# Optimization experiments

Hardware: AMD Instinct MI355X
Metric: run time of the kernel (lower is better)

The kernel has to match this reference:

```python
import jax, jax.numpy as jnp
import numpy as np
from jax import lax

H = 32   # hidden_size
L = 8    # num_layers
D_IN = 64    # lstm input_size / fc0 out
FEAT = 4096  # feature_size
T = 300      # frame_size
B = 64       # batch


def setup_inputs() -> dict:
    key = jax.random.key(0)
    ks = jax.random.split(key, 16)
    s = 0.05
    inp = {
        "x": jax.random.normal(ks[0], (B, T, FEAT), dtype=jnp.float32),
        # fc0: Linear(4096->64), ReLU, Dropout(eval), Linear(64->64)
        "W0": jax.random.normal(ks[1], (D_IN, FEAT), dtype=jnp.float32) * s,
        "b0": jax.random.normal(ks[2], (D_IN,), dtype=jnp.float32) * s,
        "W1": jax.random.normal(ks[3], (D_IN, D_IN), dtype=jnp.float32) * s,
        "b1": jax.random.normal(ks[4], (D_IN,), dtype=jnp.float32) * s,
        # LSTM params, PyTorch layout: W_ih [4H, in], W_hh [4H, H], biases [4H]
        "Wih0": jax.random.normal(ks[5], (4 * H, D_IN), dtype=jnp.float32) * s,
        "Wih": jax.random.normal(ks[6], (L - 1, 4 * H, H), dtype=jnp.float32) * s,
        "Whh": jax.random.normal(ks[7], (L, 4 * H, H), dtype=jnp.float32) * s,
        "bih": jax.random.normal(ks[8], (L, 4 * H), dtype=jnp.float32) * s,
        "bhh": jax.random.normal(ks[9], (L, 4 * H), dtype=jnp.float32) * s,
        # fc1: 32 -> 1 ; fc2: 300 -> 1
        "Wfc1": jax.random.normal(ks[10], (1, H), dtype=jnp.float32) * s,
        "bfc1": jax.random.normal(ks[11], (1,), dtype=jnp.float32) * s,
        "Wfc2": jax.random.normal(ks[12], (1, T), dtype=jnp.float32) * s,
        "bfc2": jax.random.normal(ks[13], (1,), dtype=jnp.float32) * s,
    }
    return inp


def _lstm_layer(x_seq, Wih_l, Whh_l, bih_l, bhh_l):
    # x_seq: [B, T, in] -> h_seq: [B, T, H]; PyTorch gate order i,f,g,o
    gx = jnp.einsum('bti,gi->btg', x_seq, Wih_l) + bih_l  # [B,T,4H]
    b = x_seq.shape[0]
    init = (jnp.zeros((b, H), x_seq.dtype), jnp.zeros((b, H), x_seq.dtype))

    def step(carry, gx_t):
        h, c = carry
        g = gx_t + h @ Whh_l.T + bhh_l
        i, f, gg, o = jnp.split(g, 4, axis=-1)
        c = jax.nn.sigmoid(f) * c + jax.nn.sigmoid(i) * jnp.tanh(gg)
        h = jax.nn.sigmoid(o) * jnp.tanh(c)
        return (h, c), h

    _, hs = lax.scan(step, init, jnp.swapaxes(gx, 0, 1))  # hs: [T,B,H]
    return jnp.swapaxes(hs, 0, 1)


def reference(x, W0, b0, W1, b1, Wih0, Wih, Whh, bih, bhh, Wfc1, bfc1, Wfc2, bfc2):
    # fc0 (dropout is identity in eval mode)
    h = jax.nn.relu(jnp.einsum('btf,of->bto', x, W0) + b0)
    h = jnp.einsum('bti,oi->bto', h, W1) + b1  # [B,T,64]
    # stacked LSTM, h0=c0=0
    for l in range(L):
        Wih_l = Wih0 if l == 0 else Wih[l - 1]
        h = _lstm_layer(h, Wih_l, Whh[l], bih[l], bhh[l])  # [B,T,32]
    # fc1 over hidden, squeeze, fc2 over time, squeeze
    y = jnp.einsum('bth,oh->bto', h, Wfc1)[..., 0] + bfc1[0]  # [B,T]
    y = y @ Wfc2.T + bfc2  # [B,1]
    return y[:, 0]
```

## Files before the change

kernel.cpp:

```cpp
#include <hip/hip_runtime.h>
#include <cstdint>

#define FEAT 4096
#define DIN  64
#define HS   32
#define NL   8
#define TT   300
#define BB   64
#define G4   128
#define MROWS (BB*TT)
#define KS    4
#define KSLICE (FEAT/KS)
#define BK    64
#define NCHUNK (KSLICE/BK)

typedef __bf16 bf16x8 __attribute__((ext_vector_type(8)));
typedef float  f32x4  __attribute__((ext_vector_type(4)));
typedef unsigned short u16x8 __attribute__((ext_vector_type(8)));

__device__ __forceinline__ float sigm(float x){ return __fdividef(1.f, 1.f + __expf(-x)); }
__device__ __forceinline__ float tanh_f(float x){ return __fdividef(2.f, 1.f + __expf(-2.f*x)) - 1.f; }

__device__ __forceinline__ unsigned short bf16_rne(float f){
    uint32_t u = __float_as_uint(f);
    return (unsigned short)((u + 0x7FFFu + ((u >> 16) & 1u)) >> 16);
}

__global__ __launch_bounds__(256) void w0split(const float* __restrict__ W0,
                                               unsigned short* __restrict__ wh,
                                               unsigned short* __restrict__ wl)
{
    const int i = (blockIdx.x * 256 + threadIdx.x) * 4;
    float4 v = *(const float4*)(W0 + i);
    float f[4] = {v.x, v.y, v.z, v.w};
    unsigned short hh[4], ll[4];
    #pragma unroll
    for (int j = 0; j < 4; ++j) {
        unsigned short h = bf16_rne(f[j]);
        float fh = __uint_as_float((uint32_t)h << 16);
        hh[j] = h;
        ll[j] = bf16_rne(f[j] - fh);
    }
    *(ushort4*)(wh + i) = make_ushort4(hh[0], hh[1], hh[2], hh[3]);
    *(ushort4*)(wl + i) = make_ushort4(ll[0], ll[1], ll[2], ll[3]);
}

__global__ __launch_bounds__(256, 2) void fc_gemm1(
    const float* __restrict__ x,
    const unsigned short* __restrict__ wh,
    const unsigned short* __restrict__ wl,
    float* __restrict__ part)
{
    __shared__ __align__(16) unsigned short xh[2][64][64];
    __shared__ __align__(16) unsigned short xl[2][64][64];
    __shared__ __align__(16) unsigned short wh_s[2][64][64];
    __shared__ __align__(16) unsigned short wl_s[2][64][64];

    const int t   = threadIdx.x;
    const int l   = t & 63;
    const int w   = t >> 6;
    const int rbb = (w >> 1) * 32;
    const int cbb = (w & 1) * 32;
    const int r0  = blockIdx.x * 64;
    const int kb0 = blockIdx.y * KSLICE;

    const int srow = t >> 3;
    const int sg   = t & 7;

    f32x4 acc[2][2];
    #pragma unroll
    for (int i = 0; i < 2; ++i)
        #pragma unroll
        for (int j = 0; j < 2; ++j)
            acc[i][j] = (f32x4){0.f, 0.f, 0.f, 0.f};

    float4 xr[2][2];
    uint4  w0h[2], w0l[2];

    auto LOAD = [&](int c) {
        const float* xb = x + (size_t)r0 * FEAT + kb0 + c * BK;
        xr[0][0] = *(const float4*)(xb + (size_t)srow * FEAT + sg * 8);
        xr[0][1] = *(const float4*)(xb + (size_t)srow * FEAT + sg * 8 + 4);
        xr[1][0] = *(const float4*)(xb + (size_t)(srow + 32) * FEAT + sg * 8);
        xr[1][1] = *(const float4*)(xb + (size_t)(srow + 32) * FEAT + sg * 8 + 4);
        const int wo = kb0 + c * BK + sg * 8;
        w0h[0] = *(const uint4*)(wh + (size_t)srow * FEAT + wo);
        w0h[1] = *(const uint4*)(wh + (size_t)(srow + 32) * FEAT + wo);
        w0l[0] = *(const uint4*)(wl + (size_t)srow * FEAT + wo);
        w0l[1] = *(const uint4*)(wl + (size_t)(srow + 32) * FEAT + wo);
    };

    auto STORE = [&](int c) {
        const int buf = c & 1;
        #pragma unroll
        for (int j = 0; j < 2; ++j) {
            const int row = srow + j * 32;
            const int gsw = (sg ^ (row & 7)) * 8;
            float f0[8] = {xr[j][0].x, xr[j][0].y, xr[j][0].z, xr[j][0].w,
                           xr[j][1].x, xr[j][1].y, xr[j][1].z, xr[j][1].w};
            u16x8 vh, vl;
            #pragma unroll
            for (int i = 0; i < 8; ++i) {
                uint32_t u  = __float_as_uint(f0[i]);
                uint32_t rh = (u + 0x7FFFu + ((u >> 16) & 1u)) >> 16;
                vh[i] = (unsigned short)rh;
                float fl = f0[i] - __uint_as_float(rh << 16);
                uint32_t u2 = __float_as_uint(fl);
                vl[i] = (unsigned short)((u2 + 0x7FFFu + ((u2 >> 16) & 1u)) >> 16);
            }
            *(u16x8*)&xh[buf][row][gsw] = vh;
            *(u16x8*)&xl[buf][row][gsw] = vl;
            *(uint4*)&wh_s[buf][row][gsw] = w0h[j];
            *(uint4*)&wl_s[buf][row][gsw] = w0l[j];
        }
    };

    auto COMPUTE = [&](int buf) {
        #pragma unroll
        for (int kstep = 0; kstep < 2; ++kstep) {
            const int gA = kstep * 4 + (l >> 4);
            bf16x8 Ah[2], Al[2], Bh[2], Bl[2];
            #pragma unroll
            for (int rf = 0; rf < 2; ++rf) {
                const int ra  = rbb + rf * 16 + (l & 15);
                const int off = (gA ^ (ra & 7)) * 8;
                Ah[rf] = __builtin_bit_cast(bf16x8, *(const u16x8*)&xh[buf][ra][off]);
                Al[rf] = __builtin_bit_cast(bf16x8, *(const u16x8*)&xl[buf][ra][off]);
            }
            #pragma unroll
            for (int cf = 0; cf < 2; ++cf) {
                const int cb  = cbb + cf * 16 + (l & 15);
                const int off = (gA ^ (cb & 7)) * 8;
                Bh[cf] = __builtin_bit_cast(bf16x8, *(const u16x8*)&wh_s[buf][cb][off]);
                Bl[cf] = __builtin_bit_cast(bf16x8, *(const u16x8*)&wl_s[buf][cb][off]);
            }
            #pragma unroll
            for (int rf = 0; rf < 2; ++rf)
                #pragma unroll
                for (int cf = 0; cf < 2; ++cf) {
                    acc[rf][cf] = __builtin_amdgcn_mfma_f32_16x16x32_bf16(Ah[rf], Bh[cf], acc[rf][cf], 0, 0, 0);
                    acc[rf][cf] = __builtin_amdgcn_mfma_f32_16x16x32_bf16(Al[rf], Bh[cf], acc[rf][cf], 0, 0, 0);
                    acc[rf][cf] = __builtin_amdgcn_mfma_f32_16x16x32_bf16(Ah[rf], Bl[cf], acc[rf][cf], 0, 0, 0);
                }
        }
    };

    LOAD(0);
    for (int c = 0; c < NCHUNK; ++c) {
        STORE(c);
        if (c + 1 < NCHUNK) LOAD(c + 1);
        asm volatile("s_waitcnt lgkmcnt(0)" ::: "memory");
        __builtin_amdgcn_s_barrier();
        COMPUTE(c & 1);
    }

    #pragma unroll
    for (int rf = 0; rf < 2; ++rf)
        #pragma unroll
        for (int cf = 0; cf < 2; ++cf)
            #pragma unroll
            for (int r = 0; r < 4; ++r) {
                const int row = r0 + rbb + rf * 16 + (l >> 4) * 4 + r;
                const int col = cbb + cf * 16 + (l & 15);
                part[((size_t)blockIdx.y * MROWS + row) * 64 + col] = acc[rf][cf][r];
            }
}

__global__ __launch_bounds__(256) void fc_tail(
    const float* __restrict__ part, const float* __restrict__ b0,
    const float* __restrict__ W1, const float* __restrict__ b1,
    const float* __restrict__ Wih0,
    const float* __restrict__ bih, const float* __restrict__ bhh,
    float* __restrict__ gx0)
{
    __shared__ __align__(16) float h1s[64][68];
    __shared__ __align__(16) float h2s[64][68];

    const int tid = threadIdx.x;
    const int tc  = tid & 15;
    const int tr  = tid >> 4;
    const int r0  = blockIdx.x * 64;

    {
        const int row = tid >> 2;
        const int c0  = (tid & 3) * 16;
        float4 s[4];
        #pragma unroll
        for (int i = 0; i < 4; ++i)
            s[i] = *(const float4*)(part + ((size_t)(r0 + row)) * 64 + c0 + 4 * i);
        #pragma unroll
        for (int ks = 1; ks < KS; ++ks)
            #pragma unroll
            for (int i = 0; i < 4; ++i) {
                float4 v = *(const float4*)(part + ((size_t)ks * MROWS + r0 + row) * 64 + c0 + 4 * i);
                s[i].x += v.x; s[i].y += v.y; s[i].z += v.z; s[i].w += v.w;
            }
        #pragma unroll
        for (int i = 0; i < 4; ++i) {
            float4 bv = *(const float4*)(b0 + c0 + 4 * i);
            float4 o;
            o.x = fmaxf(s[i].x + bv.x, 0.f);
            o.y = fmaxf(s[i].y + bv.y, 0.f);
            o.z = fmaxf(s[i].z + bv.z, 0.f);
            o.w = fmaxf(s[i].w + bv.w, 0.f);
            *(float4*)&h1s[row][c0 + 4 * i] = o;
        }
    }
    __syncthreads();

    float acc2[4][4] = {};
    #pragma unroll
    for (int k4 = 0; k4 < 16; ++k4) {
        const int k = k4 * 4;
        float4 a[4], wv[4];
        #pragma unroll
        for (int i = 0; i < 4; ++i) a[i] = *(const float4*)&h1s[tr * 4 + i][k];
        #pragma unroll
        for (int j = 0; j < 4; ++j) wv[j] = *(const float4*)(W1 + (size_t)(tc * 4 + j) * DIN + k);
        #pragma unroll
        for (int i = 0; i < 4; ++i)
            #pragma unroll
            for (int j = 0; j < 4; ++j)
                acc2[i][j] += a[i].x * wv[j].x + a[i].y * wv[j].y + a[i].z * wv[j].z + a[i].w * wv[j].w;
    }
    __syncthreads();
    #pragma unroll
    for (int i = 0; i < 4; ++i)
        #pragma unroll
        for (int j = 0; j < 4; ++j)
            h2s[tr * 4 + i][tc * 4 + j] = acc2[i][j] + b1[tc * 4 + j];
    __syncthreads();

    #pragma unroll
    for (int p = 0; p < 2; ++p) {
        float acc3[4][4] = {};
        #pragma unroll
        for (int k4 = 0; k4 < 16; ++k4) {
            const int k = k4 * 4;
            float4 a[4], wv[4];
            #pragma unroll
            for (int i = 0; i < 4; ++i) a[i] = *(const float4*)&h2s[tr * 4 + i][k];
            #pragma unroll
            for (int j = 0; j < 4; ++j) wv[j] = *(const float4*)(Wih0 + (size_t)(p * 64 + tc * 4 + j) * DIN + k);
            #pragma unroll
            for (int i = 0; i < 4; ++i)
                #pragma unroll
                for (int j = 0; j < 4; ++j)
                    acc3[i][j] += a[i].x * wv[j].x + a[i].y * wv[j].y + a[i].z * wv[j].z + a[i].w * wv[j].w;
        }
        const int g0 = p * 64 + tc * 4;
        #pragma unroll
        for (int i = 0; i < 4; ++i) {
            float4 ov;
            ov.x = acc3[i][0] + bih[g0 + 0] + bhh[g0 + 0];
            ov.y = acc3[i][1] + bih[g0 + 1] + bhh[g0 + 1];
            ov.z = acc3[i][2] + bih[g0 + 2] + bhh[g0 + 2];
            ov.w = acc3[i][3] + bih[g0 + 3] + bhh[g0 + 3];
            *(float4*)(gx0 + (size_t)(r0 + tr * 4 + i) * G4 + g0) = ov;
        }
    }
}

__global__ __launch_bounds__(512, 2) void lstm_all(
    const float* __restrict__ gx0,
    const float* __restrict__ Wih, const float* __restrict__ Whh,
    const float* __restrict__ bih, const float* __restrict__ bhh,
    const float* __restrict__ Wfc1, const float* __restrict__ bfc1,
    const float* __restrict__ Wfc2, const float* __restrict__ bfc2,
    float* __restrict__ out)
{
    const int b    = blockIdx.x;
    const int tid  = threadIdx.x;
    const int l    = tid >> 6;
    const int lane = tid & 63;
    const int q0   = lane;
    const int q1   = lane + 64;

    __shared__ __align__(16) float hbuf[NL][2][HS];
    __shared__ __align__(16) float gbuf[NL][G4];
    __shared__ __align__(16) float h7[TT][HS];
    __shared__ float red[NL];

    float whh0[HS], whh1[HS], wih0[HS], wih1[HS];
    {
        const float* whhl = Whh + (size_t)l * G4 * HS;
        const float* wihl = Wih + (size_t)(l > 0 ? l - 1 : 0) * G4 * HS;
        #pragma unroll
        for (int k4 = 0; k4 < 8; ++k4) {
            float4 v0 = *(const float4*)(whhl + q0 * HS + 4 * k4);
            float4 v1 = *(const float4*)(whhl + q1 * HS + 4 * k4);
            whh0[4*k4+0]=v0.x; whh0[4*k4+1]=v0.y; whh0[4*k4+2]=v0.z; whh0[4*k4+3]=v0.w;
            whh1[4*k4+0]=v1.x; whh1[4*k4+1]=v1.y; whh1[4*k4+2]=v1.z; whh1[4*k4+3]=v1.w;
            float4 u0 = *(const float4*)(wihl + q0 * HS + 4 * k4);
            float4 u1 = *(const float4*)(wihl + q1 * HS + 4 * k4);
            wih0[4*k4+0]=u0.x; wih0[4*k4+1]=u0.y; wih0[4*k4+2]=u0.z; wih0[4*k4+3]=u0.w;
            wih1[4*k4+0]=u1.x; wih1[4*k4+1]=u1.y; wih1[4*k4+2]=u1.z; wih1[4*k4+3]=u1.w;
        }
    }
    const float bias0 = (l > 0) ? (bih[l*G4 + q0] + bhh[l*G4 + q0]) : 0.f;
    const float bias1 = (l > 0) ? (bih[l*G4 + q1] + bhh[l*G4 + q1]) : 0.f;

    float c_state = 0.f;

    const float* gxb = gx0 + (size_t)b * TT * G4;
    float pf0 = 0.f, pf1 = 0.f;
    if (l == 0) { pf0 = gxb[q0]; pf1 = gxb[q1]; }

    for (int s = 0; s < TT + NL - 1; ++s) {
        const int t = s - l;
        if (0 <= t && t < TT) {
            float acc0, acc1;
            if (l == 0) {
                acc0 = pf0; acc1 = pf1;
                const int tn = t + 1;
                if (tn < TT) { pf0 = gxb[(size_t)tn * G4 + q0]; pf1 = gxb[(size_t)tn * G4 + q1]; }
            } else {
                acc0 = bias0; acc1 = bias1;
            }
            float a0a = 0.f, a0b = 0.f, a1a = 0.f, a1b = 0.f;
            if (t > 0) {
                const float4* hp = (const float4*)hbuf[l][(t - 1) & 1];
                #pragma unroll
                for (int k4 = 0; k4 < 8; ++k4) {
                    float4 v = hp[k4];
                    a0a = fmaf(whh0[4*k4+0], v.x, a0a); a0b = fmaf(whh0[4*k4+1], v.y, a0b);
                    a0a = fmaf(whh0[4*k4+2], v.z, a0a); a0b = fmaf(whh0[4*k4+3], v.w, a0b);
                    a1a = fmaf(whh1[4*k4+0], v.x, a1a); a1b = fmaf(whh1[4*k4+1], v.y, a1b);
                    a1a = fmaf(whh1[4*k4+2], v.z, a1a); a1b = fmaf(whh1[4*k4+3], v.w, a1b);
                }
            }
            if (l > 0) {
                const float4* hq = (const float4*)hbuf[l - 1][t & 1];
                #pragma unroll
                for (int k4 = 0; k4 < 8; ++k4) {
                    float4 v = hq[k4];
                    a0a = fmaf(wih0[4*k4+0], v.x, a0a); a0b = fmaf(wih0[4*k4+1], v.y, a0b);
                    a0a = fmaf(wih0[4*k4+2], v.z, a0a); a0b = fmaf(wih0[4*k4+3], v.w, a0b);
                    a1a = fmaf(wih1[4*k4+0], v.x, a1a); a1b = fmaf(wih1[4*k4+1], v.y, a1b);
                    a1a = fmaf(wih1[4*k4+2], v.z, a1a); a1b = fmaf(wih1[4*k4+3], v.w, a1b);
                }
            }
            acc0 += a0a + a0b;
            acc1 += a1a + a1b;
            gbuf[l][q0] = acc0;
            gbuf[l][q1] = acc1;
            asm volatile("s_waitcnt lgkmcnt(0)" ::: "memory");
            if (lane < HS) {
                const float ig = gbuf[l][lane];
                const float fg = gbuf[l][HS + lane];
                const float gg = gbuf[l][2*HS + lane];
                const float og = gbuf[l][3*HS + lane];
                c_state = sigm(fg) * c_state + sigm(ig) * tanh_f(gg);
                const float hv = sigm(og) * tanh_f(c_state);
                hbuf[l][t & 1][lane] = hv;
                if (l == NL - 1) h7[t][lane] = hv;
            }
        }
        __syncthreads();
    }

    float part = 0.f;
    for (int t = tid; t < TT; t += 512) {
        float st = 0.f;
        #pragma unroll
        for (int j = 0; j < HS; ++j) st = fmaf(h7[t][j], Wfc1[j], st);
        part += (st + bfc1[0]) * Wfc2[t];
    }
    #pragma unroll
    for (int off = 32; off >= 1; off >>= 1) part += __shfl_down(part, off, 64);
    if (lane == 0) red[l] = part;
    __syncthreads();
    if (tid == 0) {
        float tot = 0.f;
        #pragma unroll
        for (int w = 0; w < NL; ++w) tot += red[w];
        out[b] = tot + bfc2[0];
    }
}

extern "C" void kernel_launch(void* const* d_in, const int* in_sizes, int n_in,
                              void* d_out, int out_size, void* d_ws, size_t ws_size,
                              hipStream_t stream) {
    const float* x    = (const float*)d_in[0];
    const float* W0   = (const float*)d_in[1];
    const float* b0   = (const float*)d_in[2];
    const float* W1   = (const float*)d_in[3];
    const float* b1   = (const float*)d_in[4];
    const float* Wih0 = (const float*)d_in[5];
    const float* Wih  = (const float*)d_in[6];
    const float* Whh  = (const float*)d_in[7];
    const float* bih  = (const float*)d_in[8];
    const float* bhh  = (const float*)d_in[9];
    const float* Wfc1 = (const float*)d_in[10];
    const float* bfc1 = (const float*)d_in[11];
    const float* Wfc2 = (const float*)d_in[12];
    const float* bfc2 = (const float*)d_in[13];

    char* wsb = (char*)d_ws;
    float*          gx0 = (float*)wsb;
    unsigned short* wh  = (unsigned short*)(wsb + 9830400);
    unsigned short* wl  = (unsigned short*)(wsb + 9830400 + 524288);
    float*          prt = (float*)(wsb + 9830400 + 1048576);

    w0split <<<256, 256, 0, stream>>>(W0, wh, wl);
    fc_gemm1<<<dim3(MROWS / 64, KS), 256, 0, stream>>>(x, wh, wl, prt);
    fc_tail <<<MROWS / 64, 256, 0, stream>>>(prt, b0, W1, b1, Wih0, bih, bhh, gx0);
    lstm_all<<<BB, 512, 0, stream>>>(gx0, Wih, Whh, bih, bhh, Wfc1, bfc1, Wfc2, bfc2,
                                     (float*)d_out);
}
```

Measured before the change: 432.3 us.

## Process two timesteps per barrier in wavefront LSTM and use shuffle gate exchange

```diff
diff --git a/kernel.cpp b/kernel.cpp
--- a/kernel.cpp
+++ b/kernel.cpp
@@ -13,6 +13,7 @@
 #define KSLICE (FEAT/KS)
 #define BK    64
 #define NCHUNK (KSLICE/BK)
+#define NSUP  (TT/2 + NL - 1)
 
 typedef __bf16 bf16x8 __attribute__((ext_vector_type(8)));
 typedef float  f32x4  __attribute__((ext_vector_type(4)));
@@ -20,6 +21,13 @@
 
 __device__ __forceinline__ float sigm(float x){ return __fdividef(1.f, 1.f + __expf(-x)); }
 __device__ __forceinline__ float tanh_f(float x){ return __fdividef(2.f, 1.f + __expf(-2.f*x)) - 1.f; }
+
+__device__ __forceinline__ float2 pkfma(float2 w, float h, float2 c){
+    return make_float2(fmaf(w.x, h, c.x), fmaf(w.y, h, c.y));
+}
+__device__ __forceinline__ float2 add2(float2 a, float2 b){
+    return make_float2(a.x + b.x, a.y + b.y);
+}
 
 __device__ __forceinline__ unsigned short bf16_rne(float f){
     uint32_t u = __float_as_uint(f);
@@ -276,84 +284,139 @@
     const int q0   = lane;
     const int q1   = lane + 64;
 
-    __shared__ __align__(16) float hbuf[NL][2][HS];
-    __shared__ __align__(16) float gbuf[NL][G4];
+    __shared__ __align__(16) float hbuf[NL][2][2][HS];
     __shared__ __align__(16) float h7[TT][HS];
     __shared__ float red[NL];
 
-    float whh0[HS], whh1[HS], wih0[HS], wih1[HS];
+    float2 whh2[HS], wih2[HS];
     {
         const float* whhl = Whh + (size_t)l * G4 * HS;
         const float* wihl = Wih + (size_t)(l > 0 ? l - 1 : 0) * G4 * HS;
         #pragma unroll
-        for (int k4 = 0; k4 < 8; ++k4) {
-            float4 v0 = *(const float4*)(whhl + q0 * HS + 4 * k4);
-            float4 v1 = *(const float4*)(whhl + q1 * HS + 4 * k4);
-            whh0[4*k4+0]=v0.x; whh0[4*k4+1]=v0.y; whh0[4*k4+2]=v0.z; whh0[4*k4+3]=v0.w;
-            whh1[4*k4+0]=v1.x; whh1[4*k4+1]=v1.y; whh1[4*k4+2]=v1.z; whh1[4*k4+3]=v1.w;
-            float4 u0 = *(const float4*)(wihl + q0 * HS + 4 * k4);
-            float4 u1 = *(const float4*)(wihl + q1 * HS + 4 * k4);
-            wih0[4*k4+0]=u0.x; wih0[4*k4+1]=u0.y; wih0[4*k4+2]=u0.z; wih0[4*k4+3]=u0.w;
-            wih1[4*k4+0]=u1.x; wih1[4*k4+1]=u1.y; wih1[4*k4+2]=u1.z; wih1[4*k4+3]=u1.w;
-        }
-    }
-    const float bias0 = (l > 0) ? (bih[l*G4 + q0] + bhh[l*G4 + q0]) : 0.f;
-    const float bias1 = (l > 0) ? (bih[l*G4 + q1] + bhh[l*G4 + q1]) : 0.f;
+        for (int k = 0; k < HS; k += 4) {
+            float4 a0 = *(const float4*)(whhl + q0 * HS + k);
+            float4 a1 = *(const float4*)(whhl + q1 * HS + k);
+            whh2[k+0] = make_float2(a0.x, a1.x);
+            whh2[k+1] = make_float2(a0.y, a1.y);
+            whh2[k+2] = make_float2(a0.z, a1.z);
+            whh2[k+3] = make_float2(a0.w, a1.w);
+            float4 u0 = *(const float4*)(wihl + q0 * HS + k);
+            float4 u1 = *(const float4*)(wihl + q1 * HS + k);
+            wih2[k+0] = make_float2(u0.x, u1.x);
+            wih2[k+1] = make_float2(u0.y, u1.y);
+            wih2[k+2] = make_float2(u0.z, u1.z);
+            wih2[k+3] = make_float2(u0.w, u1.w);
+        }
+    }
+    const float2 bias2 = (l > 0)
+        ? make_float2(bih[l*G4 + q0] + bhh[l*G4 + q0], bih[l*G4 + q1] + bhh[l*G4 + q1])
+        : make_float2(0.f, 0.f);
 
     float c_state = 0.f;
 
     const float* gxb = gx0 + (size_t)b * TT * G4;
-    float pf0 = 0.f, pf1 = 0.f;
-    if (l == 0) { pf0 = gxb[q0]; pf1 = gxb[q1]; }
-
-    for (int s = 0; s < TT + NL - 1; ++s) {
-        const int t = s - l;
-        if (0 <= t && t < TT) {
-            float acc0, acc1;
+    float2 pg0 = make_float2(0.f, 0.f), pg1 = pg0;
+    if (l == 0) {
+        pg0 = make_float2(gxb[q0],      gxb[q1]);
+        pg1 = make_float2(gxb[G4 + q0], gxb[G4 + q1]);
+    }
+
+    for (int s = 0; s < NSUP; ++s) {
+        const int t0 = 2 * (s - l);
+        if (0 <= t0 && t0 < TT) {
+            float2 g0, g1;
             if (l == 0) {
-                acc0 = pf0; acc1 = pf1;
-                const int tn = t + 1;
-                if (tn < TT) { pf0 = gxb[(size_t)tn * G4 + q0]; pf1 = gxb[(size_t)tn * G4 + q1]; }
-            } else {
-                acc0 = bias0; acc1 = bias1;
-            }
-            float a0a = 0.f, a0b = 0.f, a1a = 0.f, a1b = 0.f;
-            if (t > 0) {
-                const float4* hp = (const float4*)hbuf[l][(t - 1) & 1];
+                g0 = pg0; g1 = pg1;
+                const int tn = t0 + 2;
+                if (tn < TT) {
+                    pg0 = make_float2(gxb[(size_t)tn * G4 + q0],       gxb[(size_t)tn * G4 + q1]);
+                    pg1 = make_float2(gxb[(size_t)(tn + 1) * G4 + q0], gxb[(size_t)(tn + 1) * G4 + q1]);
+                }
+            }
+
+            float2 P0[2] = {make_float2(0,0), make_float2(0,0)};
+            float2 P1[2] = {make_float2(0,0), make_float2(0,0)};
+            if (l > 0) {
+                const float4* hp0 = (const float4*)hbuf[l-1][(s-1) & 1][0];
+                const float4* hp1 = (const float4*)hbuf[l-1][(s-1) & 1][1];
                 #pragma unroll
                 for (int k4 = 0; k4 < 8; ++k4) {
-                    float4 v = hp[k4];
-                    a0a = fmaf(whh0[4*k4+0], v.x, a0a); a0b = fmaf(whh0[4*k4+1], v.y, a0b);
-                    a0a = fmaf(whh0[4*k4+2], v.z, a0a); a0b = fmaf(whh0[4*k4+3], v.w, a0b);
-                    a1a = fmaf(whh1[4*k4+0], v.x, a1a); a1b = fmaf(whh1[4*k4+1], v.y, a1b);
-                    a1a = fmaf(whh1[4*k4+2], v.z, a1a); a1b = fmaf(whh1[4*k4+3], v.w, a1b);
-                }
-            }
-            if (l > 0) {
-                const float4* hq = (const float4*)hbuf[l - 1][t & 1];
+                    float4 v = hp0[k4];
+                    P0[0] = pkfma(wih2[4*k4+0], v.x, P0[0]);
+                    P0[1] = pkfma(wih2[4*k4+1], v.y, P0[1]);
+                    P0[0] = pkfma(wih2[4*k4+2], v.z, P0[0]);
+                    P0[1] = pkfma(wih2[4*k4+3], v.w, P0[1]);
+                }
                 #pragma unroll
                 for (int k4 = 0; k4 < 8; ++k4) {
-                    float4 v = hq[k4];
-                    a0a = fmaf(wih0[4*k4+0], v.x, a0a); a0b = fmaf(wih0[4*k4+1], v.y, a0b);
-                    a0a = fmaf(wih0[4*k4+2], v.z, a0a); a0b = fmaf(wih0[4*k4+3], v.w, a0b);
-                    a1a = fmaf(wih1[4*k4+0], v.x, a1a); a1b = fmaf(wih1[4*k4+1], v.y, a1b);
-                    a1a = fmaf(wih1[4*k4+2], v.z, a1a); a1b = fmaf(wih1[4*k4+3], v.w, a1b);
-                }
-            }
-            acc0 += a0a + a0b;
-            acc1 += a1a + a1b;
-            gbuf[l][q0] = acc0;
-            gbuf[l][q1] = acc1;
-            asm volatile("s_waitcnt lgkmcnt(0)" ::: "memory");
-            if (lane < HS) {
-                const float ig = gbuf[l][lane];
-                const float fg = gbuf[l][HS + lane];
-                const float gg = gbuf[l][2*HS + lane];
-                const float og = gbuf[l][3*HS + lane];
-                c_state = sigm(fg) * c_state + sigm(ig) * tanh_f(gg);
-                const float hv = sigm(og) * tanh_f(c_state);
-                hbuf[l][t & 1][lane] = hv;
-                if (l == NL - 1) h7[t][lane] = hv;
+                    float4 v = hp1[k4];
+                    P1[0] = pkfma(wih2[4*k4+0], v.x, P1[0]);
+                    P1[1] = pkfma(wih2[4*k4+1], v.y, P1[1]);
+                    P1[0] = pkfma(wih2[4*k4+2], v.z, P1[0]);
+                    P1[1] = pkfma(wih2[4*k4+3], v.w, P1[1]);
+                }
+            }
+
+            float2 R[2] = {make_float2(0,0), make_float2(0,0)};
+            if (t0 > 0) {
+                const float4* hs = (const float4*)hbuf[l][(s-1) & 1][1];
+                #pragma unroll
+                for (int k4 = 0; k4 < 8; ++k4) {
+                    float4 v = hs[k4];
+                    R[0] = pkfma(whh2[4*k4+0], v.x, R[0]);
+                    R[1] = pkfma(whh2[4*k4+1], v.y, R[1]);
+                    R[0] = pkfma(whh2[4*k4+2], v.z, R[0]);
+                    R[1] = pkfma(whh2[4*k4+3], v.w, R[1]);
+                }
+            }
+            float2 gate = add2(add2(R[0], R[1]),
+                               (l == 0) ? g0 : add2(bias2, add2(P0[0], P0[1])));
+
+            {
+                const float sw0 = __shfl_xor(gate.x, 32, 64);
+                const float sw1 = __shfl_xor(gate.y, 32, 64);
+                const bool lo = (lane < 32);
+                const float gi = lo ? gate.x : sw0;
+                const float gf = lo ? sw0 : gate.x;
+                const float gg = lo ? gate.y : sw1;
+                const float go = lo ? sw1 : gate.y;
+                c_state = sigm(gf) * c_state + sigm(gi) * tanh_f(gg);
+                const float hv = sigm(go) * tanh_f(c_state);
+                if (lane < HS) {
+                    hbuf[l][s & 1][0][lane] = hv;
+                    if (l == NL - 1) h7[t0][lane] = hv;
+                }
+            }
+            asm volatile("s_waitcnt lgkmcnt(0)");
+
+            float2 R1[2] = {make_float2(0,0), make_float2(0,0)};
+            {
+                const float4* hs = (const float4*)hbuf[l][s & 1][0];
+                #pragma unroll
+                for (int k4 = 0; k4 < 8; ++k4) {
+                    float4 v = hs[k4];
+                    R1[0] = pkfma(whh2[4*k4+0], v.x, R1[0]);
+                    R1[1] = pkfma(whh2[4*k4+1], v.y, R1[1]);
+                    R1[0] = pkfma(whh2[4*k4+2], v.z, R1[0]);
+                    R1[1] = pkfma(whh2[4*k4+3], v.w, R1[1]);
+                }
+            }
+            float2 gate1 = add2(add2(R1[0], R1[1]),
+                                (l == 0) ? g1 : add2(bias2, add2(P1[0], P1[1])));
+            {
+                const float sw0 = __shfl_xor(gate1.x, 32, 64);
+                const float sw1 = __shfl_xor(gate1.y, 32, 64);
+                const bool lo = (lane < 32);
+                const float gi = lo ? gate1.x : sw0;
+                const float gf = lo ? sw0 : gate1.x;
+                const float gg = lo ? gate1.y : sw1;
+                const float go = lo ? sw1 : gate1.y;
+                c_state = sigm(gf) * c_state + sigm(gi) * tanh_f(gg);
+                const float hv = sigm(go) * tanh_f(c_state);
+                if (lane < HS) {
+                    hbuf[l][s & 1][1][lane] = hv;
+                    if (l == NL - 1) h7[t0 + 1][lane] = hv;
+                }
             }
         }
         __syncthreads();
```

Result: slower. 524.8 us (+21.4%).

## Assign two LSTM layers per wavefront to shorten the wavefront pipeline

Applied to the files above, without the earlier changes.

```diff
diff --git a/kernel.cpp b/kernel.cpp
--- a/kernel.cpp
+++ b/kernel.cpp
@@ -13,6 +13,8 @@
 #define KSLICE (FEAT/KS)
 #define BK    64
 #define NCHUNK (KSLICE/BK)
+#define NW    4
+#define NSUP  (TT + NW - 1)
 
 typedef __bf16 bf16x8 __attribute__((ext_vector_type(8)));
 typedef float  f32x4  __attribute__((ext_vector_type(4)));
@@ -261,7 +263,7 @@
     }
 }
 
-__global__ __launch_bounds__(512, 2) void lstm_all(
+__global__ __launch_bounds__(256, 1) void lstm_all(
     const float* __restrict__ gx0,
     const float* __restrict__ Wih, const float* __restrict__ Whh,
     const float* __restrict__ bih, const float* __restrict__ bhh,
@@ -271,96 +273,158 @@
 {
     const int b    = blockIdx.x;
     const int tid  = threadIdx.x;
-    const int l    = tid >> 6;
+    const int w    = tid >> 6;
     const int lane = tid & 63;
     const int q0   = lane;
     const int q1   = lane + 64;
+    const int lA   = 2 * w;
+    const int lB   = 2 * w + 1;
 
     __shared__ __align__(16) float hbuf[NL][2][HS];
-    __shared__ __align__(16) float gbuf[NL][G4];
     __shared__ __align__(16) float h7[TT][HS];
-    __shared__ float red[NL];
-
-    float whh0[HS], whh1[HS], wih0[HS], wih1[HS];
+    __shared__ __align__(16) float gbuf[NW][G4];
+    __shared__ float red[NW];
+
+    float whhA0[HS], whhA1[HS], wihA0[HS], wihA1[HS];
+    float whhB0[HS], whhB1[HS], wihB0[HS], wihB1[HS];
     {
-        const float* whhl = Whh + (size_t)l * G4 * HS;
-        const float* wihl = Wih + (size_t)(l > 0 ? l - 1 : 0) * G4 * HS;
+        const float* whhl = Whh + (size_t)lA * G4 * HS;
+        const float* wihl = Wih + (size_t)(lA > 0 ? lA - 1 : 0) * G4 * HS;
         #pragma unroll
         for (int k4 = 0; k4 < 8; ++k4) {
             float4 v0 = *(const float4*)(whhl + q0 * HS + 4 * k4);
             float4 v1 = *(const float4*)(whhl + q1 * HS + 4 * k4);
-            whh0[4*k4+0]=v0.x; whh0[4*k4+1]=v0.y; whh0[4*k4+2]=v0.z; whh0[4*k4+3]=v0.w;
-            whh1[4*k4+0]=v1.x; whh1[4*k4+1]=v1.y; whh1[4*k4+2]=v1.z; whh1[4*k4+3]=v1.w;
+            whhA0[4*k4+0]=v0.x; whhA0[4*k4+1]=v0.y; whhA0[4*k4+2]=v0.z; whhA0[4*k4+3]=v0.w;
+            whhA1[4*k4+0]=v1.x; whhA1[4*k4+1]=v1.y; whhA1[4*k4+2]=v1.z; whhA1[4*k4+3]=v1.w;
             float4 u0 = *(const float4*)(wihl + q0 * HS + 4 * k4);
             float4 u1 = *(const float4*)(wihl + q1 * HS + 4 * k4);
-            wih0[4*k4+0]=u0.x; wih0[4*k4+1]=u0.y; wih0[4*k4+2]=u0.z; wih0[4*k4+3]=u0.w;
-            wih1[4*k4+0]=u1.x; wih1[4*k4+1]=u1.y; wih1[4*k4+2]=u1.z; wih1[4*k4+3]=u1.w;
-        }
-    }
-    const float bias0 = (l > 0) ? (bih[l*G4 + q0] + bhh[l*G4 + q0]) : 0.f;
-    const float bias1 = (l > 0) ? (bih[l*G4 + q1] + bhh[l*G4 + q1]) : 0.f;
-
-    float c_state = 0.f;
+            wihA0[4*k4+0]=u0.x; wihA0[4*k4+1]=u0.y; wihA0[4*k4+2]=u0.z; wihA0[4*k4+3]=u0.w;
+            wihA1[4*k4+0]=u1.x; wihA1[4*k4+1]=u1.y; wihA1[4*k4+2]=u1.z; wihA1[4*k4+3]=u1.w;
+        }
+        const float* whhm = Whh + (size_t)lB * G4 * HS;
+        const float* wihm = Wih + (size_t)(lB - 1) * G4 * HS;
+        #pragma unroll
+        for (int k4 = 0; k4 < 8; ++k4) {
+            float4 v0 = *(const float4*)(whhm + q0 * HS + 4 * k4);
+            float4 v1 = *(const float4*)(whhm + q1 * HS + 4 * k4);
+            whhB0[4*k4+0]=v0.x; whhB0[4*k4+1]=v0.y; whhB0[4*k4+2]=v0.z; whhB0[4*k4+3]=v0.w;
+            whhB1[4*k4+0]=v1.x; whhB1[4*k4+1]=v1.y; whhB1[4*k4+2]=v1.z; whhB1[4*k4+3]=v1.w;
+            float4 u0 = *(const float4*)(wihm + q0 * HS + 4 * k4);
+            float4 u1 = *(const float4*)(wihm + q1 * HS + 4 * k4);
+            wihB0[4*k4+0]=u0.x; wihB0[4*k4+1]=u0.y; wihB0[4*k4+2]=u0.z; wihB0[4*k4+3]=u0.w;
+            wihB1[4*k4+0]=u1.x; wihB1[4*k4+1]=u1.y; wihB1[4*k4+2]=u1.z; wihB1[4*k4+3]=u1.w;
+        }
+    }
+    const float biasA0 = (lA > 0) ? (bih[lA*G4 + q0] + bhh[lA*G4 + q0]) : 0.f;
+    const float biasA1 = (lA > 0) ? (bih[lA*G4 + q1] + bhh[lA*G4 + q1]) : 0.f;
+    const float biasB0 = bih[lB*G4 + q0] + bhh[lB*G4 + q0];
+    const float biasB1 = bih[lB*G4 + q1] + bhh[lB*G4 + q1];
+
+    float cA = 0.f, cB = 0.f;
 
     const float* gxb = gx0 + (size_t)b * TT * G4;
     float pf0 = 0.f, pf1 = 0.f;
-    if (l == 0) { pf0 = gxb[q0]; pf1 = gxb[q1]; }
-
-    for (int s = 0; s < TT + NL - 1; ++s) {
-        const int t = s - l;
+    if (w == 0) { pf0 = gxb[q0]; pf1 = gxb[q1]; }
+
+    for (int s = 0; s < NSUP; ++s) {
+        const int t = s - w;
         if (0 <= t && t < TT) {
             float acc0, acc1;
-            if (l == 0) {
+            if (w == 0) {
                 acc0 = pf0; acc1 = pf1;
                 const int tn = t + 1;
                 if (tn < TT) { pf0 = gxb[(size_t)tn * G4 + q0]; pf1 = gxb[(size_t)tn * G4 + q1]; }
             } else {
-                acc0 = bias0; acc1 = bias1;
-            }
-            float a0a = 0.f, a0b = 0.f, a1a = 0.f, a1b = 0.f;
-            if (t > 0) {
-                const float4* hp = (const float4*)hbuf[l][(t - 1) & 1];
-                #pragma unroll
-                for (int k4 = 0; k4 < 8; ++k4) {
-                    float4 v = hp[k4];
-                    a0a = fmaf(whh0[4*k4+0], v.x, a0a); a0b = fmaf(whh0[4*k4+1], v.y, a0b);
-                    a0a = fmaf(whh0[4*k4+2], v.z, a0a); a0b = fmaf(whh0[4*k4+3], v.w, a0b);
-                    a1a = fmaf(whh1[4*k4+0], v.x, a1a); a1b = fmaf(whh1[4*k4+1], v.y, a1b);
-                    a1a = fmaf(whh1[4*k4+2], v.z, a1a); a1b = fmaf(whh1[4*k4+3], v.w, a1b);
+                acc0 = biasA0; acc1 = biasA1;
+            }
+            {
+                float a0a = 0.f, a0b = 0.f, a1a = 0.f, a1b = 0.f;
+                if (t > 0) {
+                    const float4* hp = (const float4*)hbuf[lA][(t - 1) & 1];
+                    #pragma unroll
+                    for (int k4 = 0; k4 < 8; ++k4) {
+                        float4 v = hp[k4];
+                        a0a = fmaf(whhA0[4*k4+0], v.x, a0a); a0b = fmaf(whhA0[4*k4+1], v.y, a0b);
+                        a0a = fmaf(whhA0[4*k4+2], v.z, a0a); a0b = fmaf(whhA0[4*k4+3], v.w, a0b);
+                        a1a = fmaf(whhA1[4*k4+0], v.x, a1a); a1b = fmaf(whhA1[4*k4+1], v.y, a1b);
+                        a1a = fmaf(whhA1[4*k4+2], v.z, a1a); a1b = fmaf(whhA1[4*k4+3], v.w, a1b);
+                    }
                 }
-            }
-            if (l > 0) {
-                const float4* hq = (const float4*)hbuf[l - 1][t & 1];
-                #pragma unroll
-                for (int k4 = 0; k4 < 8; ++k4) {
-                    float4 v = hq[k4];
-                    a0a = fmaf(wih0[4*k4+0], v.x, a0a); a0b = fmaf(wih0[4*k4+1], v.y, a0b);
-                    a0a = fmaf(wih0[4*k4+2], v.z, a0a); a0b = fmaf(wih0[4*k4+3], v.w, a0b);
-                    a1a = fmaf(wih1[4*k4+0], v.x, a1a); a1b = fmaf(wih1[4*k4+1], v.y, a1b);
-                    a1a = fmaf(wih1[4*k4+2], v.z, a1a); a1b = fmaf(wih1[4*k4+3], v.w, a1b);
+                if (w > 0) {
+                    const float4* hq = (const float4*)hbuf[lA - 1][t & 1];
+                    #pragma unroll
+                    for (int k4 = 0; k4 < 8; ++k4) {
+                        float4 v = hq[k4];
+                        a0a = fmaf(wihA0[4*k4+0], v.x, a0a); a0b = fmaf(wihA0[4*k4+1], v.y, a0b);
+                        a0a = fmaf(wihA0[4*k4+2], v.z, a0a); a0b = fmaf(wihA0[4*k4+3], v.w, a0b);
+                        a1a = fmaf(wihA1[4*k4+0], v.x, a1a); a1b = fmaf(wihA1[4*k4+1], v.y, a1b);
+                        a1a = fmaf(wihA1[4*k4+2], v.z, a1a); a1b = fmaf(wihA1[4*k4+3], v.w, a1b);
+                    }
                 }
-            }
-            acc0 += a0a + a0b;
-            acc1 += a1a + a1b;
-            gbuf[l][q0] = acc0;
-            gbuf[l][q1] = acc1;
+                acc0 += a0a + a0b;
+                acc1 += a1a + a1b;
+            }
+            gbuf[w][q0] = acc0;
+            gbuf[w][q1] = acc1;
             asm volatile("s_waitcnt lgkmcnt(0)" ::: "memory");
             if (lane < HS) {
-                const float ig = gbuf[l][lane];
-                const float fg = gbuf[l][HS + lane];
-                const float gg = gbuf[l][2*HS + lane];
-                const float og = gbuf[l][3*HS + lane];
-                c_state = sigm(fg) * c_state + sigm(ig) * tanh_f(gg);
-                const float hv = sigm(og) * tanh_f(c_state);
-                hbuf[l][t & 1][lane] = hv;
-                if (l == NL - 1) h7[t][lane] = hv;
+                const float ig = gbuf[w][lane];
+                const float fg = gbuf[w][HS + lane];
+                const float gg = gbuf[w][2*HS + lane];
+                const float og = gbuf[w][3*HS + lane];
+                cA = sigm(fg) * cA + sigm(ig) * tanh_f(gg);
+                const float hv = sigm(og) * tanh_f(cA);
+                hbuf[lA][t & 1][lane] = hv;
+            }
+            asm volatile("s_waitcnt lgkmcnt(0)" ::: "memory");
+
+            float b0a = biasB0, b1a = biasB1;
+            {
+                float a0a = 0.f, a0b = 0.f, a1a = 0.f, a1b = 0.f;
+                if (t > 0) {
+                    const float4* hp = (const float4*)hbuf[lB][(t - 1) & 1];
+                    #pragma unroll
+                    for (int k4 = 0; k4 < 8; ++k4) {
+                        float4 v = hp[k4];
+                        a0a = fmaf(whhB0[4*k4+0], v.x, a0a); a0b = fmaf(whhB0[4*k4+1], v.y, a0b);
+                        a0a = fmaf(whhB0[4*k4+2], v.z, a0a); a0b = fmaf(whhB0[4*k4+3], v.w, a0b);
+                        a1a = fmaf(whhB1[4*k4+0], v.x, a1a); a1b = fmaf(whhB1[4*k4+1], v.y, a1b);
+                        a1a = fmaf(whhB1[4*k4+2], v.z, a1a); a1b = fmaf(whhB1[4*k4+3], v.w, a1b);
+                    }
+                }
+                {
+                    const float4* hq = (const float4*)hbuf[lB - 1][t & 1];
+                    #pragma unroll
+                    for (int k4 = 0; k4 < 8; ++k4) {
+                        float4 v = hq[k4];
+                        a0a = fmaf(wihB0[4*k4+0], v.x, a0a); a0b = fmaf(wihB0[4*k4+1], v.y, a0b);
+                        a0a = fmaf(wihB0[4*k4+2], v.z, a0a); a0b = fmaf(wihB0[4*k4+3], v.w, a0b);
+                        a1a = fmaf(wihB1[4*k4+0], v.x, a1a); a1b = fmaf(wihB1[4*k4+1], v.y, a1b);
+                        a1a = fmaf(wihB1[4*k4+2], v.z, a1a); a1b = fmaf(wihB1[4*k4+3], v.w, a1b);
+                    }
+                }
+                b0a += a0a + a0b;
+                b1a += a1a + a1b;
+            }
+            gbuf[w][q0] = b0a;
+            gbuf[w][q1] = b1a;
+            asm volatile("s_waitcnt lgkmcnt(0)" ::: "memory");
+            if (lane < HS) {
+                const float ig = gbuf[w][lane];
+                const float fg = gbuf[w][HS + lane];
+                const float gg = gbuf[w][2*HS + lane];
+                const float og = gbuf[w][3*HS + lane];
+                cB = sigm(fg) * cB + sigm(ig) * tanh_f(gg);
+                const float hv = sigm(og) * tanh_f(cB);
+                hbuf[lB][t & 1][lane] = hv;
+                if (lB == NL - 1) h7[t][lane] = hv;
             }
         }
         __syncthreads();
     }
 
     float part = 0.f;
-    for (int t = tid; t < TT; t += 512) {
+    for (int t = tid; t < TT; t += 256) {
         float st = 0.f;
         #pragma unroll
         for (int j = 0; j < HS; ++j) st = fmaf(h7[t][j], Wfc1[j], st);
@@ -368,12 +432,12 @@
     }
     #pragma unroll
     for (int off = 32; off >= 1; off >>= 1) part += __shfl_down(part, off, 64);
-    if (lane == 0) red[l] = part;
+    if (lane == 0) red[w] = part;
     __syncthreads();
     if (tid == 0) {
         float tot = 0.f;
         #pragma unroll
-        for (int w = 0; w < NL; ++w) tot += red[w];
+        for (int v = 0; v < NW; ++v) tot += red[v];
         out[b] = tot + bfc2[0];
     }
 }
@@ -405,6 +469,6 @@
     w0split <<<256, 256, 0, stream>>>(W0, wh, wl);
     fc_gemm1<<<dim3(MROWS / 64, KS), 256, 0, stream>>>(x, wh, wl, prt);
     fc_tail <<<MROWS / 64, 256, 0, stream>>>(prt, b0, W1, b1, Wih0, bih, bhh, gx0);
-    lstm_all<<<BB, 512, 0, stream>>>(gx0, Wih, Whh, bih, bhh, Wfc1, bfc1, Wfc2, bfc2,
+    lstm_all<<<BB, 256, 0, stream>>>(gx0, Wih, Whh, bih, bhh, Wfc1, bfc1, Wfc2, bfc2,
                                      (float*)d_out);
 }
```

Result: slower. 607.0 us (+40.4%).

## Replace per-step block barrier with per-layer LDS progress flags in LSTM wavefront

Applied to the files above, without the earlier changes.

```diff
diff --git a/kernel.cpp b/kernel.cpp
--- a/kernel.cpp
+++ b/kernel.cpp
@@ -13,6 +13,7 @@
 #define KSLICE (FEAT/KS)
 #define BK    64
 #define NCHUNK (KSLICE/BK)
+#define PAR   16
 
 typedef __bf16 bf16x8 __attribute__((ext_vector_type(8)));
 typedef float  f32x4  __attribute__((ext_vector_type(4)));
@@ -276,10 +277,14 @@
     const int q0   = lane;
     const int q1   = lane + 64;
 
-    __shared__ __align__(16) float hbuf[NL][2][HS];
+    __shared__ __align__(16) float hbuf[NL][PAR][HS];
+    __shared__ __align__(16) float h7[TT][HS];
     __shared__ __align__(16) float gbuf[NL][G4];
-    __shared__ __align__(16) float h7[TT][HS];
     __shared__ float red[NL];
+    __shared__ int progress[NL];
+    #define VPROG ((volatile int*)progress)
+
+    if (tid < NL) VPROG[tid] = -1;
 
     float whh0[HS], whh1[HS], wih0[HS], wih1[HS];
     {
@@ -303,61 +308,74 @@
     float c_state = 0.f;
 
     const float* gxb = gx0 + (size_t)b * TT * G4;
-    float pf0 = 0.f, pf1 = 0.f;
-    if (l == 0) { pf0 = gxb[q0]; pf1 = gxb[q1]; }
-
-    for (int s = 0; s < TT + NL - 1; ++s) {
-        const int t = s - l;
-        if (0 <= t && t < TT) {
-            float acc0, acc1;
-            if (l == 0) {
-                acc0 = pf0; acc1 = pf1;
-                const int tn = t + 1;
-                if (tn < TT) { pf0 = gxb[(size_t)tn * G4 + q0]; pf1 = gxb[(size_t)tn * G4 + q1]; }
-            } else {
-                acc0 = bias0; acc1 = bias1;
-            }
-            float a0a = 0.f, a0b = 0.f, a1a = 0.f, a1b = 0.f;
-            if (t > 0) {
-                const float4* hp = (const float4*)hbuf[l][(t - 1) & 1];
-                #pragma unroll
-                for (int k4 = 0; k4 < 8; ++k4) {
-                    float4 v = hp[k4];
-                    a0a = fmaf(whh0[4*k4+0], v.x, a0a); a0b = fmaf(whh0[4*k4+1], v.y, a0b);
-                    a0a = fmaf(whh0[4*k4+2], v.z, a0a); a0b = fmaf(whh0[4*k4+3], v.w, a0b);
-                    a1a = fmaf(whh1[4*k4+0], v.x, a1a); a1b = fmaf(whh1[4*k4+1], v.y, a1b);
-                    a1a = fmaf(whh1[4*k4+2], v.z, a1a); a1b = fmaf(whh1[4*k4+3], v.w, a1b);
-                }
-            }
-            if (l > 0) {
-                const float4* hq = (const float4*)hbuf[l - 1][t & 1];
-                #pragma unroll
-                for (int k4 = 0; k4 < 8; ++k4) {
-                    float4 v = hq[k4];
-                    a0a = fmaf(wih0[4*k4+0], v.x, a0a); a0b = fmaf(wih0[4*k4+1], v.y, a0b);
-                    a0a = fmaf(wih0[4*k4+2], v.z, a0a); a0b = fmaf(wih0[4*k4+3], v.w, a0b);
-                    a1a = fmaf(wih1[4*k4+0], v.x, a1a); a1b = fmaf(wih1[4*k4+1], v.y, a1b);
-                    a1a = fmaf(wih1[4*k4+2], v.z, a1a); a1b = fmaf(wih1[4*k4+3], v.w, a1b);
-                }
-            }
-            acc0 += a0a + a0b;
-            acc1 += a1a + a1b;
-            gbuf[l][q0] = acc0;
-            gbuf[l][q1] = acc1;
-            asm volatile("s_waitcnt lgkmcnt(0)" ::: "memory");
-            if (lane < HS) {
-                const float ig = gbuf[l][lane];
-                const float fg = gbuf[l][HS + lane];
-                const float gg = gbuf[l][2*HS + lane];
-                const float og = gbuf[l][3*HS + lane];
-                c_state = sigm(fg) * c_state + sigm(ig) * tanh_f(gg);
-                const float hv = sigm(og) * tanh_f(c_state);
-                hbuf[l][t & 1][lane] = hv;
-                if (l == NL - 1) h7[t][lane] = hv;
-            }
-        }
-        __syncthreads();
-    }
+    float pA0 = 0.f, pA1 = 0.f, pB0 = 0.f, pB1 = 0.f;
+    if (l == 0) {
+        pA0 = gxb[q0];      pA1 = gxb[q1];
+        pB0 = gxb[G4 + q0]; pB1 = gxb[G4 + q1];
+    }
+
+    __syncthreads();
+
+    for (int t = 0; t < TT; ++t) {
+        float acc0, acc1;
+        if (l == 0) {
+            acc0 = pA0; acc1 = pA1;
+            pA0 = pB0;  pA1 = pB1;
+            const int tn = t + 2;
+            if (tn < TT) { pB0 = gxb[(size_t)tn * G4 + q0]; pB1 = gxb[(size_t)tn * G4 + q1]; }
+        } else {
+            acc0 = bias0; acc1 = bias1;
+            while (VPROG[l - 1] < t) { }
+        }
+        if (l < NL - 1 && t >= PAR) {
+            while (VPROG[l + 1] < t - PAR) { }
+        }
+        asm volatile("" ::: "memory");
+
+        float a0a = 0.f, a0b = 0.f, a1a = 0.f, a1b = 0.f;
+        if (l > 0) {
+            const float4* hq = (const float4*)hbuf[l - 1][t & (PAR - 1)];
+            #pragma unroll
+            for (int k4 = 0; k4 < 8; ++k4) {
+                float4 v = hq[k4];
+                a0a = fmaf(wih0[4*k4+0], v.x, a0a); a0b = fmaf(wih0[4*k4+1], v.y, a0b);
+                a0a = fmaf(wih0[4*k4+2], v.z, a0a); a0b = fmaf(wih0[4*k4+3], v.w, a0b);
+                a1a = fmaf(wih1[4*k4+0], v.x, a1a); a1b = fmaf(wih1[4*k4+1], v.y, a1b);
+                a1a = fmaf(wih1[4*k4+2], v.z, a1a); a1b = fmaf(wih1[4*k4+3], v.w, a1b);
+            }
+        }
+        if (t > 0) {
+            const float4* hp = (const float4*)hbuf[l][(t - 1) & (PAR - 1)];
+            #pragma unroll
+            for (int k4 = 0; k4 < 8; ++k4) {
+                float4 v = hp[k4];
+                a0a = fmaf(whh0[4*k4+0], v.x, a0a); a0b = fmaf(whh0[4*k4+1], v.y, a0b);
+                a0a = fmaf(whh0[4*k4+2], v.z, a0a); a0b = fmaf(whh0[4*k4+3], v.w, a0b);
+                a1a = fmaf(whh1[4*k4+0], v.x, a1a); a1b = fmaf(whh1[4*k4+1], v.y, a1b);
+                a1a = fmaf(whh1[4*k4+2], v.z, a1a); a1b = fmaf(whh1[4*k4+3], v.w, a1b);
+            }
+        }
+        acc0 += a0a + a0b;
+        acc1 += a1a + a1b;
+
+        gbuf[l][q0] = acc0;
+        gbuf[l][q1] = acc1;
+        asm volatile("s_waitcnt lgkmcnt(0)" ::: "memory");
+        if (lane < HS) {
+            const float ig = gbuf[l][lane];
+            const float fg = gbuf[l][HS + lane];
+            const float gg = gbuf[l][2*HS + lane];
+            const float og = gbuf[l][3*HS + lane];
+            c_state = sigm(fg) * c_state + sigm(ig) * tanh_f(gg);
+            const float hv = sigm(og) * tanh_f(c_state);
+            hbuf[l][t & (PAR - 1)][lane] = hv;
+            if (l == NL - 1) h7[t][lane] = hv;
+        }
+        asm volatile("s_waitcnt lgkmcnt(0)" ::: "memory");
+        if (lane == 0) VPROG[l] = t;
+    }
+
+    __syncthreads();
 
     float part = 0.f;
     for (int t = tid; t < TT; t += 512) {
```

New measurement: 470.8 us. 1.09x slower.
